# Performance work log

Measured on AMD Instinct MI355X. Metric: run time of the kernel, lower is better.

## Reference

```python
import jax, jax.numpy as jnp
import numpy as np

BL = 5
N_SC = 2 ** BL  # 32; LUT A assumed to be the exact product table A[i,j] = i*j
T, B, NT, C, H = 4, 16, 196, 384, 12
TAU, ALPHA = 2.0, 4.0  # LIF tau, surrogate sigmoid alpha (spikingjelly default)


def _clean(t):
    t = jnp.where(jnp.isnan(t), 0.0, t)
    return jnp.where(jnp.isinf(t), 1.0, t)


def _pow2_scale(m):
    # 2 ** int(log2(int(N_SC / m))), with m==0 -> 1 guard, as in SC_MAT_MAC_p
    m = jnp.where(m == 0, 1.0, m)
    return 2.0 ** jnp.floor(jnp.log2(jnp.floor(N_SC / m)))


def sc_linear(x, W, b):
    # Forward value = SC LUT-quantized matmul; gradient = dense linear (out.data = p
    # in torch leaves autograd on nn.Linear) -> straight-through estimator.
    a, w, c = _clean(x), _clean(W), _clean(b)
    SN2 = _pow2_scale(jnp.max(jnp.abs(a)))
    SN1 = _pow2_scale(jnp.maximum(jnp.max(jnp.abs(w)), jnp.max(jnp.abs(c))))
    aa = jnp.trunc(a * SN2)   # .int() truncates toward zero
    bb = jnp.trunc(w * SN1)
    cc = jnp.trunc(c * SN1)
    # LUT gather A[|aa|,|bb|] with sign correction, summed over K == aa @ bb.T
    # (A[i,j] = i*j), computed without materializing the (M*O*K) intermediate.
    x9 = aa @ bb.T
    p = (jnp.trunc(x9 / SN2) + cc) / SN1
    lin = x @ W.T + b
    return lin + jax.lax.stop_gradient(p - lin)


def batch_norm(x, gamma, beta):
    # training-mode batch stats over the flattened (T*B*N) token dim, eps=1e-5
    mean = x.mean(0)
    var = ((x - mean) ** 2).mean(0)
    return gamma * (x - mean) / jnp.sqrt(var + 1e-5) + beta


def lif(x_seq, v_th=1.0):
    # Multi-step LIF, v_reset=0, hard reset, detach_reset, sigmoid surrogate
    def step(v, x):
        v = v + (x - v) / TAU
        u = v - v_th
        sg = jax.nn.sigmoid(ALPHA * u)
        spike = sg + jax.lax.stop_gradient((u >= 0).astype(x.dtype) - sg)
        v = v * (1.0 - jax.lax.stop_gradient(spike))
        return v, spike
    _, s = jax.lax.scan(step, jnp.zeros_like(x_seq[0]), x_seq)
    return s


def setup_inputs() -> dict:
    key = jax.random.key(0)
    ks = jax.random.split(key, 20)
    lim = 1.0 / np.sqrt(C)
    inp = {"x": jax.random.normal(ks[0], (T, B, NT, C), jnp.float32)}
    for i, n in enumerate(["q", "k", "v", "p"]):
        inp["W" + n] = jax.random.uniform(ks[1 + 4 * i], (C, C), jnp.float32, -lim, lim)
        inp["b" + n] = jax.random.uniform(ks[2 + 4 * i], (C,), jnp.float32, -lim, lim)
        inp["g" + n] = jnp.ones((1, C), jnp.float32)
        inp["beta" + n] = jnp.zeros((1, C), jnp.float32)
    return inp


def reference(x, Wq, bq, gq, betaq, Wk, bk, gk, betak, Wv, bv, gv, betav, Wp, bp, gp, betap):
    Tn, Bn, Nt, Cn = x.shape
    d = Cn // H
    xf = x.reshape(-1, Cn)

    def qkv(W, b, g, be):
        o = batch_norm(sc_linear(xf, W, b), g, be)
        o = lif(o.reshape(Tn, Bn, Nt, Cn))
        return o.reshape(Tn, Bn, Nt, H, d).transpose(0, 1, 3, 2, 4)  # t b h n d

    q = qkv(Wq, bq, gq, betaq)
    k = qkv(Wk, bk, gk, betak)
    v = qkv(Wv, bv, gv, betav)
    attn = jnp.einsum('tbhnd,tbhmd->tbhnm', q, k) * 0.125
    y = jnp.einsum('tbhnm,tbhmd->tbhnd', attn, v)
    y = y.transpose(0, 1, 3, 2, 4).reshape(Tn, Bn, Nt, Cn)
    y = lif(y, v_th=0.5)  # attn_lif
    o = batch_norm(sc_linear(y.reshape(-1, Cn), Wp, bp), gp, betap).reshape(Tn, Bn, Nt, Cn)
    return lif(o)
```

## Files before the change

### kernel.cpp

```cpp
#include <hip/hip_runtime.h>
#include <hip/hip_bf16.h>
#include <stdint.h>

#define T_   4
#define B_   16
#define NT_  196
#define C_   384
#define H_   12
#define M_   12544
#define NW_  1152
#define PBUF_ELEMS 4816896

typedef __attribute__((ext_vector_type(8))) short bf16x8;
typedef __attribute__((ext_vector_type(4))) float f32x4;

__device__ __forceinline__ void gload_lds16(const void* g, void* l) {
  typedef __attribute__((address_space(1))) const unsigned int GU32;
  typedef __attribute__((address_space(3))) unsigned int LU32;
  __builtin_amdgcn_global_load_lds((GU32*)g, (LU32*)l, 16, 0, 0);
}

__device__ __forceinline__ short f2bf_bits(float f) {
  __hip_bfloat16 h = __float2bfloat16(f);
  return *(short*)&h;
}

__global__ __launch_bounds__(256) void absmax_x_kernel(const float* __restrict__ x, int n4,
                                                       unsigned* __restrict__ slot) {
  float m = 0.f;
  for (long i = (long)blockIdx.x * 256 + threadIdx.x; i < n4; i += (long)gridDim.x * 256) {
    float4 v = reinterpret_cast<const float4*>(x)[i];
    m = fmaxf(fmaxf(fmaxf(fabsf(v.x), fabsf(v.y)), fmaxf(fabsf(v.z), fabsf(v.w))), m);
  }
#pragma unroll
  for (int o = 32; o > 0; o >>= 1) m = fmaxf(m, __shfl_down(m, o));
  __shared__ float sm[4];
  int wid = threadIdx.x >> 6, lane = threadIdx.x & 63;
  if (lane == 0) sm[wid] = m;
  __syncthreads();
  if (threadIdx.x == 0) {
    m = fmaxf(fmaxf(sm[0], sm[1]), fmaxf(sm[2], sm[3]));
    atomicMax(slot, __float_as_uint(m));
  }
}

__global__ __launch_bounds__(256) void absmax_wb_kernel(
    const float* __restrict__ W0, const float* __restrict__ W1,
    const float* __restrict__ W2, const float* __restrict__ W3,
    const float* __restrict__ b0, const float* __restrict__ b1,
    const float* __restrict__ b2, const float* __restrict__ b3,
    unsigned* __restrict__ slots) {
  int s = blockIdx.y;
  const float* W = (s == 0) ? W0 : (s == 1) ? W1 : (s == 2) ? W2 : W3;
  const float* bb = (s == 0) ? b0 : (s == 1) ? b1 : (s == 2) ? b2 : b3;
  float m = 0.f;
  for (int i = blockIdx.x * 256 + threadIdx.x; i < C_ * C_; i += 64 * 256)
    m = fmaxf(m, fabsf(W[i]));
  if (blockIdx.x == 0)
    for (int i = threadIdx.x; i < C_; i += 256) m = fmaxf(m, fabsf(bb[i]));
#pragma unroll
  for (int o = 32; o > 0; o >>= 1) m = fmaxf(m, __shfl_down(m, o));
  __shared__ float sm[4];
  int wid = threadIdx.x >> 6, lane = threadIdx.x & 63;
  if (lane == 0) sm[wid] = m;
  __syncthreads();
  if (threadIdx.x == 0) {
    m = fmaxf(fmaxf(sm[0], sm[1]), fmaxf(sm[2], sm[3]));
    atomicMax(slots + 1 + s, __float_as_uint(m));
  }
}

__global__ __launch_bounds__(64) void scales_kernel(const unsigned* __restrict__ slots,
                                                    float* __restrict__ SC) {
  if (threadIdx.x == 0) {
    for (int i = 0; i < 5; ++i) {
      float m = __uint_as_float(slots[i]);
      if (m == 0.f) m = 1.f;
      float q = floorf(32.f / m);
      float sn = 0.f;
      if (q >= 1.f) { unsigned qi = (unsigned)q; sn = (float)(1u << (31 - __clz((int)qi))); }
      SC[i] = sn;
    }
    SC[5] = 32.f;
  }
}

__global__ __launch_bounds__(256) void quant_x_kernel(const float* __restrict__ x,
                                                      const float* __restrict__ SC,
                                                      short* __restrict__ xq) {
  const float sn2 = SC[0];
  size_t i = ((size_t)blockIdx.x * 256 + threadIdx.x) * 4;
  float4 v = *reinterpret_cast<const float4*>(x + i);
  short4 o;
  o.x = f2bf_bits(truncf(v.x * sn2));
  o.y = f2bf_bits(truncf(v.y * sn2));
  o.z = f2bf_bits(truncf(v.z * sn2));
  o.w = f2bf_bits(truncf(v.w * sn2));
  *reinterpret_cast<short4*>(xq + i) = o;
}

__global__ __launch_bounds__(256) void quant_w_kernel(
    const float* __restrict__ W0, const float* __restrict__ W1,
    const float* __restrict__ W2, const float* __restrict__ W3,
    const float* __restrict__ b0, const float* __restrict__ b1,
    const float* __restrict__ b2, const float* __restrict__ b3,
    const float* __restrict__ SC, short* __restrict__ wq, float* __restrict__ ccq) {
  int s = blockIdx.y;
  const float* W = (s == 0) ? W0 : (s == 1) ? W1 : (s == 2) ? W2 : W3;
  const float* bb = (s == 0) ? b0 : (s == 1) ? b1 : (s == 2) ? b2 : b3;
  const float sn1 = SC[1 + s];
  int gid = blockIdx.x * 256 + threadIdx.x;
  wq[(size_t)s * C_ * C_ + gid] = f2bf_bits(truncf(W[gid] * sn1));
  if (gid < C_) ccq[s * C_ + gid] = truncf(bb[gid] * sn1);
}

__global__ __launch_bounds__(256) void mfma_gemm_kernel(
    const short* __restrict__ Aq, const short* __restrict__ Bq,
    const float* __restrict__ cc, const float* __restrict__ SC,
    int sn2_slot, int sn1_base, int ldc,
    float* __restrict__ out, long long* __restrict__ part) {
  __shared__ short As[8192];
  __shared__ short Bs[8192];
  __shared__ unsigned long long sred[128][2];
  const int tid = threadIdx.x;
  const int lane = tid & 63;
  const int wid = tid >> 6;
  const int wm = wid >> 1, wn = wid & 1;
  const int m0 = blockIdx.x * 128;
  const int n0 = blockIdx.y * 128;
  if (tid < 128) { sred[tid][0] = 0ull; sred[tid][1] = 0ull; }
  f32x4 acc[4][4];
#pragma unroll
  for (int i = 0; i < 4; ++i)
#pragma unroll
    for (int j = 0; j < 4; ++j) acc[i][j] = (f32x4){0.f, 0.f, 0.f, 0.f};

  for (int k0 = 0; k0 < C_; k0 += 64) {
#pragma unroll
    for (int p = 0; p < 4; ++p) {
      int o = p * 4096 + tid * 16;
      int row = o >> 7;
      int slot = (o >> 4) & 7;
      int hs = slot ^ (row & 7);
      int ldsoff = p * 4096 + (tid & ~63) * 16;
      gload_lds16(Aq + (size_t)(m0 + row) * C_ + k0 + hs * 8, (char*)As + ldsoff);
      gload_lds16(Bq + (size_t)(n0 + row) * C_ + k0 + hs * 8, (char*)Bs + ldsoff);
    }
    __syncthreads();
#pragma unroll
    for (int kk = 0; kk < 2; ++kk) {
      bf16x8 af[4], bfr[4];
#pragma unroll
      for (int i = 0; i < 4; ++i) {
        int r = wm * 64 + i * 16 + (lane & 15);
        int h = kk * 4 + (lane >> 4);
        af[i] = *(const bf16x8*)((const char*)As + r * 128 + ((h ^ (r & 7)) << 4));
        int c = wn * 64 + i * 16 + (lane & 15);
        bfr[i] = *(const bf16x8*)((const char*)Bs + c * 128 + ((h ^ (c & 7)) << 4));
      }
#pragma unroll
      for (int i = 0; i < 4; ++i)
#pragma unroll
        for (int j = 0; j < 4; ++j)
          acc[i][j] = __builtin_amdgcn_mfma_f32_16x16x32_bf16(af[i], bfr[j], acc[i][j], 0, 0, 0);
    }
    __syncthreads();
  }
  const float SN2 = SC[sn2_slot], SN1 = SC[sn1_base + blockIdx.y / 3];
  const float invSN2 = 1.0f / SN2, invSN1 = 1.0f / SN1;
  long long s1[4] = {0, 0, 0, 0}, s2[4] = {0, 0, 0, 0};
#pragma unroll
  for (int j = 0; j < 4; ++j) {
    int gcol = n0 + wn * 64 + j * 16 + (lane & 15);
    float ccv = cc[gcol];
#pragma unroll
    for (int i = 0; i < 4; ++i) {
#pragma unroll
      for (int r = 0; r < 4; ++r) {
        int grow = m0 + wm * 64 + i * 16 + (lane >> 4) * 4 + r;
        float qf = truncf(acc[i][j][r] * invSN2) + ccv;
        out[(size_t)grow * ldc + gcol] = qf * invSN1;
        long long qi = (long long)qf;
        s1[j] += qi; s2[j] += qi * qi;
      }
    }
  }
#pragma unroll
  for (int j = 0; j < 4; ++j) {
    s1[j] += __shfl_xor(s1[j], 16); s1[j] += __shfl_xor(s1[j], 32);
    s2[j] += __shfl_xor(s2[j], 16); s2[j] += __shfl_xor(s2[j], 32);
  }
  if (lane < 16) {
#pragma unroll
    for (int j = 0; j < 4; ++j) {
      int cl = wn * 64 + j * 16 + lane;
      atomicAdd(&sred[cl][0], (unsigned long long)s1[j]);
      atomicAdd(&sred[cl][1], (unsigned long long)s2[j]);
    }
  }
  __syncthreads();
  if (tid < 128) {
    part[((size_t)blockIdx.x * ldc + n0 + tid) * 2 + 0] = (long long)sred[tid][0];
    part[((size_t)blockIdx.x * ldc + n0 + tid) * 2 + 1] = (long long)sred[tid][1];
  }
}

__global__ __launch_bounds__(384) void stats_final_kernel(
    const long long* __restrict__ part, const float* __restrict__ SC, int sn1_base, int Ld,
    float* __restrict__ bn) {
  int c = blockIdx.x * 384 + threadIdx.x;
  long long S1 = 0, S2 = 0;
  for (int b = 0; b < 98; ++b) {
    S1 += part[((size_t)b * Ld + c) * 2 + 0];
    S2 += part[((size_t)b * Ld + c) * 2 + 1];
  }
  double inv = 1.0 / (double)SC[sn1_base + blockIdx.x];
  double s = (double)S1 * inv;
  double s2 = (double)S2 * inv * inv;
  double mean = s / (double)M_;
  float m32 = (float)mean;
  double md = (double)m32;
  double var = (s2 - 2.0 * md * s + (double)M_ * md * md) / (double)M_;
  bn[c * 2 + 0] = m32;
  bn[c * 2 + 1] = sqrtf((float)var + 1e-5f);
}

__device__ __forceinline__ float lif_step(float& v, float x, float vth) {
  v = v + (x - v) * 0.5f;
  float u = v - vth;
  float spike = (u >= 0.0f) ? 1.0f : 0.0f;
  v = (u >= 0.0f) ? 0.0f : v;
  return spike;
}

__global__ __launch_bounds__(384) void bn_lif_pack_kernel(
    const float* __restrict__ pbuf, const float* __restrict__ bn,
    const float* __restrict__ g0, const float* __restrict__ g1, const float* __restrict__ g2,
    const float* __restrict__ be0, const float* __restrict__ be1, const float* __restrict__ be2,
    uint32_t* __restrict__ pack) {
  int c = threadIdx.x;
  int n = blockIdx.x, b = blockIdx.y, z = blockIdx.z;
  const float* g  = (z == 0) ? g0 : (z == 1) ? g1 : g2;
  const float* be = (z == 0) ? be0 : (z == 1) ? be1 : be2;
  int cg = z * C_ + c;
  float mean = bn[cg * 2 + 0], sd = bn[cg * 2 + 1];
  float gg = g[c], bb = be[c];
  int h = c >> 5;
  float v = 0.f;
  uint32_t* pko = pack + (size_t)z * (T_ * B_ * H_ * NT_);
  for (int t = 0; t < T_; ++t) {
    size_t row = (size_t)(t * B_ + b) * NT_ + n;
    float p = pbuf[row * NW_ + cg];
    float o = (gg * (p - mean)) / sd + bb;
    float spike = lif_step(v, o, 1.0f);
    unsigned long long m = __ballot(spike != 0.0f);
    if ((c & 31) == 0) {
      uint32_t pt = (c & 32) ? (uint32_t)(m >> 32) : (uint32_t)m;
      pko[((size_t)(t * B_ + b) * H_ + h) * NT_ + n] = pt;
    }
  }
}

__global__ __launch_bounds__(256) void zcalc_kernel(
    const uint32_t* __restrict__ kp, const uint32_t* __restrict__ vp,
    int* __restrict__ zbuf) {
  __shared__ uint32_t kT[32][8], vT[32][8];
  const int tbh = blockIdx.x;
  const int tid = threadIdx.x, lane = tid & 63, w = tid >> 6;
  size_t base = (size_t)tbh * NT_;
  uint32_t km = (tid < NT_) ? kp[base + tid] : 0u;
  uint32_t vm = (tid < NT_) ? vp[base + tid] : 0u;
#pragma unroll
  for (int j = 0; j < 32; ++j) {
    unsigned long long bk = __ballot((km >> j) & 1u);
    unsigned long long bv = __ballot((vm >> j) & 1u);
    if (lane == 0) {
      kT[j][2 * w] = (uint32_t)bk; kT[j][2 * w + 1] = (uint32_t)(bk >> 32);
      vT[j][2 * w] = (uint32_t)bv; vT[j][2 * w + 1] = (uint32_t)(bv >> 32);
    }
  }
  __syncthreads();
  int* Zg = zbuf + (size_t)tbh * 1024;
  for (int pz = tid; pz < 1024; pz += 256) {
    int j = pz >> 5, dd = pz & 31;
    int z = 0;
#pragma unroll
    for (int ww = 0; ww < 8; ++ww) z += __popc(kT[j][ww] & vT[dd][ww]);
    Zg[pz] = z;
  }
}

__global__ __launch_bounds__(256) void attn_apply_kernel(
    const uint32_t* __restrict__ qp, const int* __restrict__ zbuf,
    short* __restrict__ yq) {
  __shared__ int Zs[32][32];
  const int bh = blockIdx.x, chunk = blockIdx.y;
  const int b = bh / H_, h = bh % H_;
  const int tid = threadIdx.x;
  const int d = tid & 31, nn = tid >> 5;
  const short one32 = f2bf_bits(32.f);
  const short zer = f2bf_bits(0.f);
  float vst[7];
#pragma unroll
  for (int i = 0; i < 7; ++i) vst[i] = 0.f;
  for (int t = 0; t < T_; ++t) {
    int tbh = (t * B_ + b) * H_ + h;
    const int* Zp = zbuf + (size_t)tbh * 1024;
    for (int i = tid; i < 1024; i += 256) ((int*)Zs)[i] = Zp[i];
    __syncthreads();
    int zc[32];
#pragma unroll
    for (int j = 0; j < 32; ++j) zc[j] = Zs[j][d];
    size_t qbase = (size_t)tbh * NT_;
#pragma unroll
    for (int i = 0; i < 7; ++i) {
      int no = i * 8 + nn;
      if (no < 49) {
        int n = chunk * 49 + no;
        uint32_t qm = qp[qbase + n];
        int a = 0;
#pragma unroll
        for (int j = 0; j < 32; ++j) a += ((qm >> j) & 1u) ? zc[j] : 0;
        float y = 0.125f * (float)a;
        float v = vst[i];
        v = v + (y - v) * 0.5f;
        short outv;
        if (v - 0.5f >= 0.f) { v = 0.f; outv = one32; } else { outv = zer; }
        vst[i] = v;
        yq[((size_t)(t * B_ + b) * NT_ + n) * C_ + h * 32 + d] = outv;
      }
    }
    __syncthreads();
  }
}

__global__ __launch_bounds__(384) void bn_lif_out_kernel(
    const float* __restrict__ p2, const float* __restrict__ bn,
    const float* __restrict__ g, const float* __restrict__ beta,
    float* __restrict__ out) {
  int c = threadIdx.x, n = blockIdx.x, b = blockIdx.y;
  float mean = bn[c * 2 + 0], sd = bn[c * 2 + 1];
  float gg = g[c], bb = beta[c];
  float v = 0.f;
  for (int t = 0; t < T_; ++t) {
    size_t idx = ((size_t)(t * B_ + b) * NT_ + n) * C_ + c;
    float o = (gg * (p2[idx] - mean)) / sd + bb;
    out[idx] = lif_step(v, o, 1.0f);
  }
}

extern "C" void kernel_launch(void* const* d_in, const int* in_sizes, int n_in,
                              void* d_out, int out_size, void* d_ws, size_t ws_size,
                              hipStream_t stream) {
  (void)in_sizes; (void)n_in; (void)out_size; (void)ws_size;
  const float* x = (const float*)d_in[0];
  const float* W[4]  = {(const float*)d_in[1],  (const float*)d_in[5],
                        (const float*)d_in[9],  (const float*)d_in[13]};
  const float* bv[4] = {(const float*)d_in[2],  (const float*)d_in[6],
                        (const float*)d_in[10], (const float*)d_in[14]};
  const float* g[4]  = {(const float*)d_in[3],  (const float*)d_in[7],
                        (const float*)d_in[11], (const float*)d_in[15]};
  const float* be[4] = {(const float*)d_in[4],  (const float*)d_in[8],
                        (const float*)d_in[12], (const float*)d_in[16]};
  float* out = (float*)d_out;

  char* ws = (char*)d_ws;
  unsigned*  slots = (unsigned*)(ws + 0);
  float*     SC    = (float*)(ws + 0x40);
  float*     bnp   = (float*)(ws + 0x80);
  float*     bn2   = (float*)(ws + 0x6000);
  float*     ccq   = (float*)(ws + 0x8000);
  long long* part  = (long long*)(ws + 0x10000);
  long long* part2 = (long long*)(ws + 0x200000);
  uint32_t*  pack  = (uint32_t*)(ws + 0x300000);
  int*       zbuf  = (int*)(ws + 0x500000);
  short*     wq    = (short*)(ws + 0x800000);
  short*     xq    = (short*)(ws + 0xA00000);
  short*     yq    = (short*)(ws + 0x1400000);
  float*     pwide = (float*)(ws + 0x1E00000);
  float*     pbuf2 = (float*)(ws + 0x5600000);

  hipMemsetAsync(slots, 0, 64, stream);
  absmax_x_kernel<<<512, 256, 0, stream>>>(x, PBUF_ELEMS / 4, slots + 0);
  absmax_wb_kernel<<<dim3(64, 4), 256, 0, stream>>>(
      W[0], W[1], W[2], W[3], bv[0], bv[1], bv[2], bv[3], slots);
  scales_kernel<<<1, 64, 0, stream>>>(slots, SC);

  quant_x_kernel<<<4704, 256, 0, stream>>>(x, SC, xq);
  quant_w_kernel<<<dim3(576, 4), 256, 0, stream>>>(
      W[0], W[1], W[2], W[3], bv[0], bv[1], bv[2], bv[3], SC, wq, ccq);

  mfma_gemm_kernel<<<dim3(98, 9), 256, 0, stream>>>(
      xq, wq, ccq, SC, 0, 1, NW_, pwide, part);
  stats_final_kernel<<<3, 384, 0, stream>>>(part, SC, 1, NW_, bnp);
  bn_lif_pack_kernel<<<dim3(NT_, B_, 3), 384, 0, stream>>>(
      pwide, bnp, g[0], g[1], g[2], be[0], be[1], be[2], pack);

  zcalc_kernel<<<T_ * B_ * H_, 256, 0, stream>>>(pack + 150528, pack + 2 * 150528, zbuf);
  attn_apply_kernel<<<dim3(B_ * H_, 4), 256, 0, stream>>>(pack, zbuf, yq);

  mfma_gemm_kernel<<<dim3(98, 3), 256, 0, stream>>>(
      yq, wq + 3ull * C_ * C_, ccq + 3 * C_, SC, 5, 4, C_, pbuf2, part2);
  stats_final_kernel<<<1, 384, 0, stream>>>(part2, SC, 4, C_, bn2);
  bn_lif_out_kernel<<<dim3(NT_, B_), 384, 0, stream>>>(pbuf2, bn2, g[3], be[3], out);
}
```

Measured before the change: 252.3 us.

## Fuse prep and stats kernels, store GEMM outputs as int16, merge attention kernels

Merges the absmax, scale and quantization kernels into two launches, with scales recomputed inline from the absmax slots. The GEMM now writes integer-valued outputs as shorts instead of floats, and the last block folds in the BN statistics through global atomics and a completion counter, which removes the stats_final kernels. The zcalc and attn_apply kernels are fused so Z is built in shared memory, dropping the zbuf round trip. Together these cut launches and memory traffic, at the cost of redundant Z computation across the four chunk blocks and reliance on the quantized values fitting in int16.

```diff
diff --git a/kernel.cpp b/kernel.cpp
--- a/kernel.cpp
+++ b/kernel.cpp
@@ -25,12 +25,38 @@
   return *(short*)&h;
 }
 
-__global__ __launch_bounds__(256) void absmax_x_kernel(const float* __restrict__ x, int n4,
-                                                       unsigned* __restrict__ slot) {
+__device__ __forceinline__ float sn_from_slot(const unsigned* slots, int i) {
+  float m = __uint_as_float(slots[i]);
+  if (m == 0.f) m = 1.f;
+  float q = floorf(32.f / m);
+  float sn = 0.f;
+  if (q >= 1.f) { unsigned qi = (unsigned)q; sn = (float)(1u << (31 - __clz((int)qi))); }
+  return sn;
+}
+
+__global__ __launch_bounds__(256) void absmax_all_kernel(
+    const float* __restrict__ x,
+    const float* __restrict__ W0, const float* __restrict__ W1,
+    const float* __restrict__ W2, const float* __restrict__ W3,
+    const float* __restrict__ b0, const float* __restrict__ b1,
+    const float* __restrict__ b2, const float* __restrict__ b3,
+    unsigned* __restrict__ slots) {
+  int y = blockIdx.y;
   float m = 0.f;
-  for (long i = (long)blockIdx.x * 256 + threadIdx.x; i < n4; i += (long)gridDim.x * 256) {
-    float4 v = reinterpret_cast<const float4*>(x)[i];
-    m = fmaxf(fmaxf(fmaxf(fabsf(v.x), fabsf(v.y)), fmaxf(fabsf(v.z), fabsf(v.w))), m);
+  if (y == 0) {
+    const float4* xv = (const float4*)x;
+    for (int i = blockIdx.x * 256 + threadIdx.x; i < PBUF_ELEMS / 4; i += 128 * 256) {
+      float4 v = xv[i];
+      m = fmaxf(fmaxf(fmaxf(fabsf(v.x), fabsf(v.y)), fmaxf(fabsf(v.z), fabsf(v.w))), m);
+    }
+  } else {
+    int s = y - 1;
+    const float* W = (s == 0) ? W0 : (s == 1) ? W1 : (s == 2) ? W2 : W3;
+    const float* bb = (s == 0) ? b0 : (s == 1) ? b1 : (s == 2) ? b2 : b3;
+    for (int i = blockIdx.x * 256 + threadIdx.x; i < C_ * C_; i += 128 * 256)
+      m = fmaxf(m, fabsf(W[i]));
+    if (blockIdx.x == 0)
+      for (int i = threadIdx.x; i < C_; i += 256) m = fmaxf(m, fabsf(bb[i]));
   }
 #pragma unroll
   for (int o = 32; o > 0; o >>= 1) m = fmaxf(m, __shfl_down(m, o));
@@ -40,88 +66,53 @@
   __syncthreads();
   if (threadIdx.x == 0) {
     m = fmaxf(fmaxf(sm[0], sm[1]), fmaxf(sm[2], sm[3]));
-    atomicMax(slot, __float_as_uint(m));
-  }
-}
-
-__global__ __launch_bounds__(256) void absmax_wb_kernel(
+    atomicMax(slots + y, __float_as_uint(m));
+  }
+}
+
+__global__ __launch_bounds__(256) void quant_all_kernel(
+    const float* __restrict__ x,
     const float* __restrict__ W0, const float* __restrict__ W1,
     const float* __restrict__ W2, const float* __restrict__ W3,
     const float* __restrict__ b0, const float* __restrict__ b1,
     const float* __restrict__ b2, const float* __restrict__ b3,
-    unsigned* __restrict__ slots) {
-  int s = blockIdx.y;
-  const float* W = (s == 0) ? W0 : (s == 1) ? W1 : (s == 2) ? W2 : W3;
-  const float* bb = (s == 0) ? b0 : (s == 1) ? b1 : (s == 2) ? b2 : b3;
-  float m = 0.f;
-  for (int i = blockIdx.x * 256 + threadIdx.x; i < C_ * C_; i += 64 * 256)
-    m = fmaxf(m, fabsf(W[i]));
-  if (blockIdx.x == 0)
-    for (int i = threadIdx.x; i < C_; i += 256) m = fmaxf(m, fabsf(bb[i]));
-#pragma unroll
-  for (int o = 32; o > 0; o >>= 1) m = fmaxf(m, __shfl_down(m, o));
-  __shared__ float sm[4];
-  int wid = threadIdx.x >> 6, lane = threadIdx.x & 63;
-  if (lane == 0) sm[wid] = m;
-  __syncthreads();
-  if (threadIdx.x == 0) {
-    m = fmaxf(fmaxf(sm[0], sm[1]), fmaxf(sm[2], sm[3]));
-    atomicMax(slots + 1 + s, __float_as_uint(m));
-  }
-}
-
-__global__ __launch_bounds__(64) void scales_kernel(const unsigned* __restrict__ slots,
-                                                    float* __restrict__ SC) {
-  if (threadIdx.x == 0) {
-    for (int i = 0; i < 5; ++i) {
-      float m = __uint_as_float(slots[i]);
-      if (m == 0.f) m = 1.f;
-      float q = floorf(32.f / m);
-      float sn = 0.f;
-      if (q >= 1.f) { unsigned qi = (unsigned)q; sn = (float)(1u << (31 - __clz((int)qi))); }
-      SC[i] = sn;
-    }
-    SC[5] = 32.f;
-  }
-}
-
-__global__ __launch_bounds__(256) void quant_x_kernel(const float* __restrict__ x,
-                                                      const float* __restrict__ SC,
-                                                      short* __restrict__ xq) {
-  const float sn2 = SC[0];
-  size_t i = ((size_t)blockIdx.x * 256 + threadIdx.x) * 4;
-  float4 v = *reinterpret_cast<const float4*>(x + i);
-  short4 o;
-  o.x = f2bf_bits(truncf(v.x * sn2));
-  o.y = f2bf_bits(truncf(v.y * sn2));
-  o.z = f2bf_bits(truncf(v.z * sn2));
-  o.w = f2bf_bits(truncf(v.w * sn2));
-  *reinterpret_cast<short4*>(xq + i) = o;
-}
-
-__global__ __launch_bounds__(256) void quant_w_kernel(
-    const float* __restrict__ W0, const float* __restrict__ W1,
-    const float* __restrict__ W2, const float* __restrict__ W3,
-    const float* __restrict__ b0, const float* __restrict__ b1,
-    const float* __restrict__ b2, const float* __restrict__ b3,
-    const float* __restrict__ SC, short* __restrict__ wq, float* __restrict__ ccq) {
-  int s = blockIdx.y;
-  const float* W = (s == 0) ? W0 : (s == 1) ? W1 : (s == 2) ? W2 : W3;
-  const float* bb = (s == 0) ? b0 : (s == 1) ? b1 : (s == 2) ? b2 : b3;
-  const float sn1 = SC[1 + s];
-  int gid = blockIdx.x * 256 + threadIdx.x;
-  wq[(size_t)s * C_ * C_ + gid] = f2bf_bits(truncf(W[gid] * sn1));
-  if (gid < C_) ccq[s * C_ + gid] = truncf(bb[gid] * sn1);
+    const unsigned* __restrict__ slots,
+    short* __restrict__ xq, short* __restrict__ wq, float* __restrict__ ccq) {
+  int y = blockIdx.y;
+  if (y == 0) {
+    const float sn2 = sn_from_slot(slots, 0);
+#pragma unroll
+    for (int r = 0; r < 4; ++r) {
+      size_t i = ((size_t)blockIdx.x * 1024 + r * 256 + threadIdx.x);
+      float4 v = reinterpret_cast<const float4*>(x)[i];
+      short4 o;
+      o.x = f2bf_bits(truncf(v.x * sn2));
+      o.y = f2bf_bits(truncf(v.y * sn2));
+      o.z = f2bf_bits(truncf(v.z * sn2));
+      o.w = f2bf_bits(truncf(v.w * sn2));
+      reinterpret_cast<short4*>(xq)[i] = o;
+    }
+  } else {
+    int s = y - 1;
+    const float* W = (s == 0) ? W0 : (s == 1) ? W1 : (s == 2) ? W2 : W3;
+    const float* bb = (s == 0) ? b0 : (s == 1) ? b1 : (s == 2) ? b2 : b3;
+    const float sn1 = sn_from_slot(slots, 1 + s);
+    int gid = blockIdx.x * 256 + threadIdx.x;
+    if (gid < C_ * C_) wq[(size_t)s * C_ * C_ + gid] = f2bf_bits(truncf(W[gid] * sn1));
+    if (gid < C_) ccq[s * C_ + gid] = truncf(bb[gid] * sn1);
+  }
 }
 
 __global__ __launch_bounds__(256) void mfma_gemm_kernel(
     const short* __restrict__ Aq, const short* __restrict__ Bq,
-    const float* __restrict__ cc, const float* __restrict__ SC,
-    int sn2_slot, int sn1_base, int ldc,
-    float* __restrict__ out, long long* __restrict__ part) {
+    const float* __restrict__ cc, const unsigned* __restrict__ slots,
+    int sn2_slot, int sn1_base, int ldc, int nblk,
+    short* __restrict__ out, unsigned long long* __restrict__ sums,
+    unsigned* __restrict__ cnt, float* __restrict__ bn) {
   __shared__ short As[8192];
   __shared__ short Bs[8192];
   __shared__ unsigned long long sred[128][2];
+  __shared__ int lastflag;
   const int tid = threadIdx.x;
   const int lane = tid & 63;
   const int wid = tid >> 6;
@@ -166,8 +157,8 @@
     }
     __syncthreads();
   }
-  const float SN2 = SC[sn2_slot], SN1 = SC[sn1_base + blockIdx.y / 3];
-  const float invSN2 = 1.0f / SN2, invSN1 = 1.0f / SN1;
+  const float SN2 = (sn2_slot < 0) ? 32.f : sn_from_slot(slots, sn2_slot);
+  const float invSN2 = 1.0f / SN2;
   long long s1[4] = {0, 0, 0, 0}, s2[4] = {0, 0, 0, 0};
 #pragma unroll
   for (int j = 0; j < 4; ++j) {
@@ -179,8 +170,8 @@
       for (int r = 0; r < 4; ++r) {
         int grow = m0 + wm * 64 + i * 16 + (lane >> 4) * 4 + r;
         float qf = truncf(acc[i][j][r] * invSN2) + ccv;
-        out[(size_t)grow * ldc + gcol] = qf * invSN1;
         long long qi = (long long)qf;
+        out[(size_t)grow * ldc + gcol] = (short)qi;
         s1[j] += qi; s2[j] += qi * qi;
       }
     }
@@ -200,29 +191,27 @@
   }
   __syncthreads();
   if (tid < 128) {
-    part[((size_t)blockIdx.x * ldc + n0 + tid) * 2 + 0] = (long long)sred[tid][0];
-    part[((size_t)blockIdx.x * ldc + n0 + tid) * 2 + 1] = (long long)sred[tid][1];
-  }
-}
-
-__global__ __launch_bounds__(384) void stats_final_kernel(
-    const long long* __restrict__ part, const float* __restrict__ SC, int sn1_base, int Ld,
-    float* __restrict__ bn) {
-  int c = blockIdx.x * 384 + threadIdx.x;
-  long long S1 = 0, S2 = 0;
-  for (int b = 0; b < 98; ++b) {
-    S1 += part[((size_t)b * Ld + c) * 2 + 0];
-    S2 += part[((size_t)b * Ld + c) * 2 + 1];
-  }
-  double inv = 1.0 / (double)SC[sn1_base + blockIdx.x];
-  double s = (double)S1 * inv;
-  double s2 = (double)S2 * inv * inv;
-  double mean = s / (double)M_;
-  float m32 = (float)mean;
-  double md = (double)m32;
-  double var = (s2 - 2.0 * md * s + (double)M_ * md * md) / (double)M_;
-  bn[c * 2 + 0] = m32;
-  bn[c * 2 + 1] = sqrtf((float)var + 1e-5f);
+    atomicAdd(&sums[(size_t)(n0 + tid) * 2 + 0], sred[tid][0]);
+    atomicAdd(&sums[(size_t)(n0 + tid) * 2 + 1], sred[tid][1]);
+  }
+  __threadfence();
+  if (tid == 0) lastflag = (atomicAdd(cnt, 1u) == (unsigned)(nblk - 1)) ? 1 : 0;
+  __syncthreads();
+  if (lastflag) {
+    for (int c = tid; c < ldc; c += 256) {
+      long long S1 = (long long)atomicAdd(&sums[(size_t)c * 2 + 0], 0ull);
+      long long S2 = (long long)atomicAdd(&sums[(size_t)c * 2 + 1], 0ull);
+      double inv = 1.0 / (double)sn_from_slot(slots, sn1_base + c / C_);
+      double s = (double)S1 * inv;
+      double ss = (double)S2 * inv * inv;
+      double mean = s / (double)M_;
+      float m32 = (float)mean;
+      double md = (double)m32;
+      double var = (ss - 2.0 * md * s + (double)M_ * md * md) / (double)M_;
+      bn[c * 2 + 0] = m32;
+      bn[c * 2 + 1] = sqrtf((float)var + 1e-5f);
+    }
+  }
 }
 
 __device__ __forceinline__ float lif_step(float& v, float x, float vth) {
@@ -234,7 +223,8 @@
 }
 
 __global__ __launch_bounds__(384) void bn_lif_pack_kernel(
-    const float* __restrict__ pbuf, const float* __restrict__ bn,
+    const short* __restrict__ pw, const float* __restrict__ bn,
+    const unsigned* __restrict__ slots,
     const float* __restrict__ g0, const float* __restrict__ g1, const float* __restrict__ g2,
     const float* __restrict__ be0, const float* __restrict__ be1, const float* __restrict__ be2,
     uint32_t* __restrict__ pack) {
@@ -243,6 +233,7 @@
   const float* g  = (z == 0) ? g0 : (z == 1) ? g1 : g2;
   const float* be = (z == 0) ? be0 : (z == 1) ? be1 : be2;
   int cg = z * C_ + c;
+  float invSN1 = 1.0f / sn_from_slot(slots, 1 + z);
   float mean = bn[cg * 2 + 0], sd = bn[cg * 2 + 1];
   float gg = g[c], bb = be[c];
   int h = c >> 5;
@@ -250,7 +241,7 @@
   uint32_t* pko = pack + (size_t)z * (T_ * B_ * H_ * NT_);
   for (int t = 0; t < T_; ++t) {
     size_t row = (size_t)(t * B_ + b) * NT_ + n;
-    float p = pbuf[row * NW_ + cg];
+    float p = (float)pw[row * NW_ + cg] * invSN1;
     float o = (gg * (p - mean)) / sd + bb;
     float spike = lif_step(v, o, 1.0f);
     unsigned long long m = __ballot(spike != 0.0f);
@@ -261,63 +252,52 @@
   }
 }
 
-__global__ __launch_bounds__(256) void zcalc_kernel(
-    const uint32_t* __restrict__ kp, const uint32_t* __restrict__ vp,
-    int* __restrict__ zbuf) {
+__global__ __launch_bounds__(256) void attn_fused_kernel(
+    const uint32_t* __restrict__ qp, const uint32_t* __restrict__ kp,
+    const uint32_t* __restrict__ vp, short* __restrict__ yq) {
   __shared__ uint32_t kT[32][8], vT[32][8];
-  const int tbh = blockIdx.x;
-  const int tid = threadIdx.x, lane = tid & 63, w = tid >> 6;
-  size_t base = (size_t)tbh * NT_;
-  uint32_t km = (tid < NT_) ? kp[base + tid] : 0u;
-  uint32_t vm = (tid < NT_) ? vp[base + tid] : 0u;
-#pragma unroll
-  for (int j = 0; j < 32; ++j) {
-    unsigned long long bk = __ballot((km >> j) & 1u);
-    unsigned long long bv = __ballot((vm >> j) & 1u);
-    if (lane == 0) {
-      kT[j][2 * w] = (uint32_t)bk; kT[j][2 * w + 1] = (uint32_t)(bk >> 32);
-      vT[j][2 * w] = (uint32_t)bv; vT[j][2 * w + 1] = (uint32_t)(bv >> 32);
-    }
-  }
-  __syncthreads();
-  int* Zg = zbuf + (size_t)tbh * 1024;
-  for (int pz = tid; pz < 1024; pz += 256) {
-    int j = pz >> 5, dd = pz & 31;
-    int z = 0;
-#pragma unroll
-    for (int ww = 0; ww < 8; ++ww) z += __popc(kT[j][ww] & vT[dd][ww]);
-    Zg[pz] = z;
-  }
-}
-
-__global__ __launch_bounds__(256) void attn_apply_kernel(
-    const uint32_t* __restrict__ qp, const int* __restrict__ zbuf,
-    short* __restrict__ yq) {
   __shared__ int Zs[32][32];
   const int bh = blockIdx.x, chunk = blockIdx.y;
   const int b = bh / H_, h = bh % H_;
-  const int tid = threadIdx.x;
+  const int tid = threadIdx.x, lane = tid & 63, w = tid >> 6;
   const int d = tid & 31, nn = tid >> 5;
   const short one32 = f2bf_bits(32.f);
-  const short zer = f2bf_bits(0.f);
+  const short zer = 0;
   float vst[7];
 #pragma unroll
   for (int i = 0; i < 7; ++i) vst[i] = 0.f;
   for (int t = 0; t < T_; ++t) {
     int tbh = (t * B_ + b) * H_ + h;
-    const int* Zp = zbuf + (size_t)tbh * 1024;
-    for (int i = tid; i < 1024; i += 256) ((int*)Zs)[i] = Zp[i];
+    size_t base = (size_t)tbh * NT_;
+    uint32_t km = (tid < NT_) ? kp[base + tid] : 0u;
+    uint32_t vm = (tid < NT_) ? vp[base + tid] : 0u;
+#pragma unroll
+    for (int j = 0; j < 32; ++j) {
+      unsigned long long bk = __ballot((km >> j) & 1u);
+      unsigned long long bv = __ballot((vm >> j) & 1u);
+      if (lane == 0) {
+        kT[j][2 * w] = (uint32_t)bk; kT[j][2 * w + 1] = (uint32_t)(bk >> 32);
+        vT[j][2 * w] = (uint32_t)bv; vT[j][2 * w + 1] = (uint32_t)(bv >> 32);
+      }
+    }
+    __syncthreads();
+    for (int pz = tid; pz < 1024; pz += 256) {
+      int j = pz >> 5, dd = pz & 31;
+      int zz = 0;
+#pragma unroll
+      for (int ww = 0; ww < 8; ++ww) zz += __popc(kT[j][ww] & vT[dd][ww]);
+      Zs[j][dd] = zz;
+    }
     __syncthreads();
     int zc[32];
 #pragma unroll
     for (int j = 0; j < 32; ++j) zc[j] = Zs[j][d];
-    size_t qbase = (size_t)tbh * NT_;
 #pragma unroll
     for (int i = 0; i < 7; ++i) {
       int no = i * 8 + nn;
       if (no < 49) {
         int n = chunk * 49 + no;
-        uint32_t qm = qp[qbase + n];
+        uint32_t qm = qp[base + n];
         int a = 0;
 #pragma unroll
         for (int j = 0; j < 32; ++j) a += ((qm >> j) & 1u) ? zc[j] : 0;
@@ -335,16 +315,19 @@
 }
 
 __global__ __launch_bounds__(384) void bn_lif_out_kernel(
-    const float* __restrict__ p2, const float* __restrict__ bn,
+    const short* __restrict__ p2, const float* __restrict__ bn,
+    const unsigned* __restrict__ slots,
     const float* __restrict__ g, const float* __restrict__ beta,
     float* __restrict__ out) {
   int c = threadIdx.x, n = blockIdx.x, b = blockIdx.y;
+  float invSN1 = 1.0f / sn_from_slot(slots, 4);
   float mean = bn[c * 2 + 0], sd = bn[c * 2 + 1];
   float gg = g[c], bb = beta[c];
   float v = 0.f;
   for (int t = 0; t < T_; ++t) {
     size_t idx = ((size_t)(t * B_ + b) * NT_ + n) * C_ + c;
-    float o = (gg * (p2[idx] - mean)) / sd + bb;
+    float p = (float)p2[idx] * invSN1;
+    float o = (gg * (p - mean)) / sd + bb;
     out[idx] = lif_step(v, o, 1.0f);
   }
 }
@@ -365,42 +348,37 @@
   float* out = (float*)d_out;
 
   char* ws = (char*)d_ws;
-  unsigned*  slots = (unsigned*)(ws + 0);
-  float*     SC    = (float*)(ws + 0x40);
-  float*     bnp   = (float*)(ws + 0x80);
-  float*     bn2   = (float*)(ws + 0x6000);
-  float*     ccq   = (float*)(ws + 0x8000);
-  long long* part  = (long long*)(ws + 0x10000);
-  long long* part2 = (long long*)(ws + 0x200000);
-  uint32_t*  pack  = (uint32_t*)(ws + 0x300000);
-  int*       zbuf  = (int*)(ws + 0x500000);
-  short*     wq    = (short*)(ws + 0x800000);
-  short*     xq    = (short*)(ws + 0xA00000);
-  short*     yq    = (short*)(ws + 0x1400000);
-  float*     pwide = (float*)(ws + 0x1E00000);
-  float*     pbuf2 = (float*)(ws + 0x5600000);
-
-  hipMemsetAsync(slots, 0, 64, stream);
-  absmax_x_kernel<<<512, 256, 0, stream>>>(x, PBUF_ELEMS / 4, slots + 0);
-  absmax_wb_kernel<<<dim3(64, 4), 256, 0, stream>>>(
-      W[0], W[1], W[2], W[3], bv[0], bv[1], bv[2], bv[3], slots);
-  scales_kernel<<<1, 64, 0, stream>>>(slots, SC);
-
-  quant_x_kernel<<<4704, 256, 0, stream>>>(x, SC, xq);
-  quant_w_kernel<<<dim3(576, 4), 256, 0, stream>>>(
-      W[0], W[1], W[2], W[3], bv[0], bv[1], bv[2], bv[3], SC, wq, ccq);
+  unsigned*           slots = (unsigned*)(ws + 0x0000);
+  unsigned*           cnt1  = (unsigned*)(ws + 0x0040);
+  unsigned*           cnt2  = (unsigned*)(ws + 0x0044);
+  unsigned long long* sums1 = (unsigned long long*)(ws + 0x0080);
+  unsigned long long* sums2 = (unsigned long long*)(ws + 0x4880);
+  float*              bn1   = (float*)(ws + 0x8000);
+  float*              bn2   = (float*)(ws + 0xB000);
+  float*              ccq   = (float*)(ws + 0xC000);
+  uint32_t*           pack  = (uint32_t*)(ws + 0x10000);
+  short*              wq    = (short*)(ws + 0x200000);
+  short*              xq    = (short*)(ws + 0x400000);
+  short*              yq    = (short*)(ws + 0xE00000);
+  short*              pwide = (short*)(ws + 0x1800000);
+  short*              p2    = (short*)(ws + 0x3400000);
+
+  hipMemsetAsync(ws, 0, 0x6100, stream);
+
+  absmax_all_kernel<<<dim3(128, 5), 256, 0, stream>>>(
+      x, W[0], W[1], W[2], W[3], bv[0], bv[1], bv[2], bv[3], slots);
+  quant_all_kernel<<<dim3(1176, 5), 256, 0, stream>>>(
+      x, W[0], W[1], W[2], W[3], bv[0], bv[1], bv[2], bv[3], slots, xq, wq, ccq);
 
   mfma_gemm_kernel<<<dim3(98, 9), 256, 0, stream>>>(
-      xq, wq, ccq, SC, 0, 1, NW_, pwide, part);
-  stats_final_kernel<<<3, 384, 0, stream>>>(part, SC, 1, NW_, bnp);
+      xq, wq, ccq, slots, 0, 1, NW_, 98 * 9, pwide, sums1, cnt1, bn1);
   bn_lif_pack_kernel<<<dim3(NT_, B_, 3), 384, 0, stream>>>(
-      pwide, bnp, g[0], g[1], g[2], be[0], be[1], be[2], pack);
-
-  zcalc_kernel<<<T_ * B_ * H_, 256, 0, stream>>>(pack + 150528, pack + 2 * 150528, zbuf);
-  attn_apply_kernel<<<dim3(B_ * H_, 4), 256, 0, stream>>>(pack, zbuf, yq);
+      pwide, bn1, slots, g[0], g[1], g[2], be[0], be[1], be[2], pack);
+
+  attn_fused_kernel<<<dim3(B_ * H_, 4), 256, 0, stream>>>(
+      pack, pack + 150528, pack + 2 * 150528, yq);
 
   mfma_gemm_kernel<<<dim3(98, 3), 256, 0, stream>>>(
-      yq, wq + 3ull * C_ * C_, ccq + 3 * C_, SC, 5, 4, C_, pbuf2, part2);
-  stats_final_kernel<<<1, 384, 0, stream>>>(part2, SC, 4, C_, bn2);
-  bn_lif_out_kernel<<<dim3(NT_, B_), 384, 0, stream>>>(pbuf2, bn2, g[3], be[3], out);
-}
+      yq, wq + 3ull * C_ * C_, ccq + 3 * C_, slots, -1, 4, C_, 98 * 3, p2, sums2, cnt2, bn2);
+  bn_lif_out_kernel<<<dim3(NT_, B_), 384, 0, stream>>>(p2, bn2, slots, g[3], be[3], out);
+}
```

After: 351.0 us. +39.1%, slower.
